# Performance work log

Measured on AMD Instinct MI355X. Metric: run time of the kernel, lower is better.

Reference implementation:

```python
import jax, jax.numpy as jnp
import numpy as np


def setup_inputs() -> dict:
    key = jax.random.key(0)
    k1, k2 = jax.random.split(key)
    B, N, F = 16, 4096, 512
    S, K = 8, 1024          # splits, symbols per codebook
    D = F // S              # sub-vector dim
    x = jax.random.normal(k1, (B, N, F), dtype=jnp.float32)
    # torch init: uniform(-1/symbols, 1/symbols)
    codebooks = jax.random.uniform(k2, (S, K, D), dtype=jnp.float32,
                                   minval=-1.0 / K, maxval=1.0 / K)
    return {"x": x, "codebooks": codebooks}


def reference(x, codebooks):
    B, N, F = x.shape
    S, K, D = codebooks.shape
    xs = x.reshape(B, N, S, D)                       # split into S chunks
    x2 = jnp.sum(xs * xs, axis=-1, keepdims=True)    # [B,N,S,1]
    c2 = jnp.sum(codebooks * codebooks, axis=-1)     # [S,K]
    xc = jnp.einsum('bnsd,skd->bnsk', xs, codebooks)
    dist = x2 + c2[None, None] - 2.0 * xc            # [B,N,S,K]
    idx = jnp.argmin(dist, axis=-1)                  # [B,N,S]
    # gather chosen code vectors per split -> [B,N,S,D]
    sym = codebooks[jnp.arange(S)[None, None, :], idx]
    sg = jax.lax.stop_gradient
    # straight-through quantized output
    quant = (xs + sg(sym - xs)).reshape(B, N, F)
    # per-split mse (mean over B,N,D of each chunk), summed over splits
    dev = (jnp.sum(jnp.mean((sym - sg(xs)) ** 2, axis=(0, 1, 3)))
           + 0.25 * jnp.sum(jnp.mean((xs - sg(sym)) ** 2, axis=(0, 1, 3))))
    return quant, dev
```

## Files before the change

### kernel.cpp

```cpp
#include <hip/hip_runtime.h>
#include <cstdint>

constexpr int Bv = 16, Nv = 4096, Fv = 512, Sv = 8, Kv = 1024, Dv = 64;
constexpr int Mv = Bv * Nv;
#define BDIM 512
constexpr int RG = 4;

using bf16x8 = __attribute__((ext_vector_type(8))) short;
using f32x4  = __attribute__((ext_vector_type(4))) float;
typedef unsigned short u16;
typedef unsigned int u32;

__device__ __forceinline__ u16 bf16rne(float f) {
  union { float f; u32 u; } v; v.f = f;
  u32 u = v.u + 0x7FFFu + ((v.u >> 16) & 1u);
  return (u16)(u >> 16);
}

__device__ __forceinline__ u32 cvtpk(float lo, float hi) {
  u32 r;
  asm("v_cvt_pk_bf16_f32 %0, %1, %2" : "=v"(r) : "v"(lo), "v"(hi));
  return r;
}

__device__ __forceinline__ void gload_lds16(const void* g, void* lds) {
  __builtin_amdgcn_global_load_lds(
      (const __attribute__((address_space(1))) void*)g,
      (__attribute__((address_space(3))) void*)lds, 16, 0, 0);
}
__device__ __forceinline__ void gload_lds4(const void* g, void* lds) {
  __builtin_amdgcn_global_load_lds(
      (const __attribute__((address_space(1))) void*)g,
      (__attribute__((address_space(3))) void*)lds, 4, 0, 0);
}

__global__ void prep_kernel(const float* __restrict__ cb, u16* __restrict__ swz,
                            float* __restrict__ c2m) {
  int idx = blockIdx.x * 256 + threadIdx.x;
  int cw = idx & (Kv - 1);
  const float4* src = (const float4*)(cb + (size_t)idx * Dv);
  float v[64];
  float s2 = 0.f;
#pragma unroll
  for (int i = 0; i < 16; ++i) {
    float4 f = src[i];
    v[i * 4 + 0] = f.x; v[i * 4 + 1] = f.y; v[i * 4 + 2] = f.z; v[i * 4 + 3] = f.w;
    s2 += f.x * f.x + f.y * f.y + f.z * f.z + f.w * f.w;
  }
  c2m[idx] = -0.5f * s2;
  uint4* out = (uint4*)(swz + (size_t)idx * Dv);
#pragma unroll
  for (int slot = 0; slot < 8; ++slot) {
    int slotp = slot ^ (cw & 7);
    u32 w[4];
#pragma unroll
    for (int p = 0; p < 4; ++p)
      w[p] = (u32)bf16rne(v[slot * 8 + p * 2]) | ((u32)bf16rne(v[slot * 8 + p * 2 + 1]) << 16);
    uint4 pk; pk.x = w[0]; pk.y = w[1]; pk.z = w[2]; pk.w = w[3];
    out[slotp] = pk;
  }
}

__global__ __launch_bounds__(BDIM, 2) void pq_mfma(
    const float* __restrict__ x, const float* __restrict__ cb,
    const u16* __restrict__ swz, const float* __restrict__ c2m_g,
    float* __restrict__ quant, float* __restrict__ devpart) {
  __shared__ __attribute__((aligned(16))) u16 cw_lds[Kv * Dv];
  __shared__ __attribute__((aligned(16))) float c2_lds[Kv];

  const int tid = threadIdx.x;
  const int s = blockIdx.x & 7;
  const int chunk = blockIdx.x >> 3;
  const int wave = tid >> 6, lane = tid & 63;
  const int l15 = lane & 15, lg = lane >> 4;
  const int slotp0 = lg ^ (l15 & 7);
  const int slotp1 = (4 + lg) ^ (l15 & 7);

  const u16* swz_s = swz + (size_t)s * Kv * Dv;
#pragma unroll
  for (int it = 0; it < 16; ++it)
    gload_lds16(swz_s + (size_t)(it * BDIM + tid) * 8,
                &cw_lds[(it * BDIM + (tid & ~63)) * 8]);
#pragma unroll
  for (int it = 0; it < 2; ++it)
    gload_lds4(c2m_g + s * Kv + it * BDIM + tid,
               &c2_lds[it * BDIM + (tid & ~63)]);

  float4 xr[RG][4];
  {
    const float* xb = x + (size_t)(chunk * 1024 + wave * 64) * Fv + s * Dv;
#pragma unroll
    for (int rg = 0; rg < RG; ++rg) {
      const float* xp = xb + (size_t)(rg * 16 + l15) * Fv + lg * 8;
      xr[rg][0] = *(const float4*)xp;
      xr[rg][1] = *(const float4*)(xp + 4);
      xr[rg][2] = *(const float4*)(xp + 32);
      xr[rg][3] = *(const float4*)(xp + 36);
    }
  }

  __syncthreads();

  const u16* r0 = cw_lds + l15 * Dv + slotp0 * 8;
  const u16* r1 = cw_lds + l15 * Dv + slotp1 * 8;

  const u32 lgr0 = (u32)(lg * 4), lgr1 = lgr0 | 1u, lgr2 = lgr0 | 2u, lgr3 = lgr0 | 3u;
  float devx2 = 0.f, bvsum = 0.f;

#pragma unroll 1
  for (int u = 0; u < 2; ++u) {
    const int rowu = chunk * 1024 + u * 512 + wave * 64;

    bf16x8 xf[RG][2];
#pragma unroll
    for (int rg = 0; rg < RG; ++rg) {
#pragma unroll
      for (int h = 0; h < 2; ++h) {
        float4 f0 = xr[rg][h * 2], f1 = xr[rg][h * 2 + 1];
        devx2 += f0.x * f0.x + f0.y * f0.y + f0.z * f0.z + f0.w * f0.w
               + f1.x * f1.x + f1.y * f1.y + f1.z * f1.z + f1.w * f1.w;
        union { u32 w[4]; bf16x8 v; } cvt;
        cvt.w[0] = cvtpk(f0.x, f0.y);
        cvt.w[1] = cvtpk(f0.z, f0.w);
        cvt.w[2] = cvtpk(f1.x, f1.y);
        cvt.w[3] = cvtpk(f1.z, f1.w);
        xf[rg][h] = cvt.v;
      }
    }

    float bv[RG];
#pragma unroll
    for (int rg = 0; rg < RG; ++rg) bv[rg] = -3.0e38f;

    bf16x8 aA0, aA1, aB0, aB1, aC0, aC1;
    f32x4 c2A, c2B, c2C;
    f32x4 acc[RG];

    auto readA = [&](int t) {
      aA0 = *(const bf16x8*)(r0 + t * 16 * Dv);
      aA1 = *(const bf16x8*)(r1 + t * 16 * Dv);
      c2A = *(const f32x4*)&c2_lds[t * 16 + lg * 4];
    };
    auto readB = [&](int t) {
      aB0 = *(const bf16x8*)(r0 + t * 16 * Dv);
      aB1 = *(const bf16x8*)(r1 + t * 16 * Dv);
      c2B = *(const f32x4*)&c2_lds[t * 16 + lg * 4];
    };
    auto readC = [&](int t) {
      aC0 = *(const bf16x8*)(r0 + t * 16 * Dv);
      aC1 = *(const bf16x8*)(r1 + t * 16 * Dv);
      c2C = *(const f32x4*)&c2_lds[t * 16 + lg * 4];
    };
    auto mfmaA = [&]() {
      __builtin_amdgcn_s_setprio(1);
#pragma unroll
      for (int rg = 0; rg < RG; ++rg)
        acc[rg] = __builtin_amdgcn_mfma_f32_16x16x32_bf16(aA0, xf[rg][0], c2A, 0, 0, 0);
#pragma unroll
      for (int rg = 0; rg < RG; ++rg)
        acc[rg] = __builtin_amdgcn_mfma_f32_16x16x32_bf16(aA1, xf[rg][1], acc[rg], 0, 0, 0);
      __builtin_amdgcn_s_setprio(0);
    };
    auto mfmaB = [&]() {
      __builtin_amdgcn_s_setprio(1);
#pragma unroll
      for (int rg = 0; rg < RG; ++rg)
        acc[rg] = __builtin_amdgcn_mfma_f32_16x16x32_bf16(aB0, xf[rg][0], c2B, 0, 0, 0);
#pragma unroll
      for (int rg = 0; rg < RG; ++rg)
        acc[rg] = __builtin_amdgcn_mfma_f32_16x16x32_bf16(aB1, xf[rg][1], acc[rg], 0, 0, 0);
      __builtin_amdgcn_s_setprio(0);
    };
    auto mfmaC = [&]() {
      __builtin_amdgcn_s_setprio(1);
#pragma unroll
      for (int rg = 0; rg < RG; ++rg)
        acc[rg] = __builtin_amdgcn_mfma_f32_16x16x32_bf16(aC0, xf[rg][0], c2C, 0, 0, 0);
#pragma unroll
      for (int rg = 0; rg < RG; ++rg)
        acc[rg] = __builtin_amdgcn_mfma_f32_16x16x32_bf16(aC1, xf[rg][1], acc[rg], 0, 0, 0);
      __builtin_amdgcn_s_setprio(0);
    };
    auto proc = [&](u32 tb) {
#pragma unroll
      for (int rg = 0; rg < RG; ++rg) {
        float p0 = __builtin_bit_cast(float, (__builtin_bit_cast(u32, acc[rg][0]) | tb) | lgr0);
        float p1 = __builtin_bit_cast(float, (__builtin_bit_cast(u32, acc[rg][1]) | tb) | lgr1);
        float p2 = __builtin_bit_cast(float, (__builtin_bit_cast(u32, acc[rg][2]) | tb) | lgr2);
        float p3 = __builtin_bit_cast(float, (__builtin_bit_cast(u32, acc[rg][3]) | tb) | lgr3);
        float m = fmaxf(fmaxf(p0, p1), p2);
        bv[rg] = fmaxf(fmaxf(m, p3), bv[rg]);
      }
    };

    readA(0); readB(1); readC(2);
#pragma unroll 1
    for (int k = 0; k < 20; ++k) {
      const int t = 3 * k;
      mfmaA(); readA(t + 3); proc((u32)(t << 4));
      mfmaB(); readB(t + 4); proc((u32)((t + 1) << 4));
      mfmaC(); readC(t + 5); proc((u32)((t + 2) << 4));
    }
    mfmaA(); readA(63); proc(60u << 4);
    mfmaB(); proc(61u << 4);
    mfmaC(); proc(62u << 4);
    mfmaA(); proc(63u << 4);

#pragma unroll
    for (int rg = 0; rg < RG; ++rg) {
      float b = bv[rg];
      b = fmaxf(b, __shfl_xor(b, 16, 64));
      b = fmaxf(b, __shfl_xor(b, 32, 64));
      bv[rg] = b;
      bvsum += b;
    }

    if (u == 0) {
      const float* xb = x + (size_t)(chunk * 1024 + 512 + wave * 64) * Fv + s * Dv;
#pragma unroll
      for (int rg = 0; rg < RG; ++rg) {
        const float* xp = xb + (size_t)(rg * 16 + l15) * Fv + lg * 8;
        xr[rg][0] = *(const float4*)xp;
        xr[rg][1] = *(const float4*)(xp + 4);
        xr[rg][2] = *(const float4*)(xp + 32);
        xr[rg][3] = *(const float4*)(xp + 36);
      }
    }

    const float* cbs = cb + (size_t)s * Kv * Dv;
    float* qbase = quant + (size_t)rowu * Fv + s * Dv;
#pragma unroll
    for (int i = 0; i < 16; ++i) {
      int rl = i * 4 + lg;
      int kk = __shfl(__builtin_bit_cast(int, bv[i >> 2]), 4 * (i & 3) + lg, 64) & 1023;
      f32x4 v = *(const f32x4*)(cbs + (size_t)kk * Dv + l15 * 4);
      __builtin_nontemporal_store(v, (f32x4*)(qbase + (size_t)rl * Fv + l15 * 4));
    }
  }

#pragma unroll
  for (int m = 1; m <= 32; m <<= 1) devx2 += __shfl_xor(devx2, m, 64);
#pragma unroll
  for (int m = 1; m <= 8; m <<= 1) bvsum += __shfl_xor(bvsum, m, 64);
  if (lane == 0)
    devpart[(size_t)blockIdx.x * 8 + wave] = devx2 - 2.f * bvsum;
}

__global__ void dev_reduce(const float* __restrict__ part, float* __restrict__ out) {
  __shared__ float sred[256];
  int tid = threadIdx.x;
  float s = 0.f;
  for (int i = tid; i < 4096; i += 256) s += part[i];
  sred[tid] = s;
  __syncthreads();
  for (int off = 128; off > 0; off >>= 1) {
    if (tid < off) sred[tid] += sred[tid + off];
    __syncthreads();
  }
  if (tid == 0) out[0] = sred[0] * (1.25f / 4194304.0f);
}

extern "C" void kernel_launch(void* const* d_in, const int* in_sizes, int n_in,
                              void* d_out, int out_size, void* d_ws, size_t ws_size,
                              hipStream_t stream) {
  const float* x = (const float*)d_in[0];
  const float* cb = (const float*)d_in[1];
  float* quant = (float*)d_out;
  float* dev = quant + (size_t)Mv * Fv;

  u16* swz = (u16*)d_ws;
  float* c2m = (float*)(swz + (size_t)Sv * Kv * Dv);
  float* part = c2m + Sv * Kv;

  prep_kernel<<<(Sv * Kv) / 256, 256, 0, stream>>>(cb, swz, c2m);
  pq_mfma<<<512, BDIM, 0, stream>>>(x, cb, swz, c2m, quant, part);
  dev_reduce<<<1, 256, 0, stream>>>(part, dev);
}
```

Baseline: 97.97 us.

## Double-buffer MFMA accumulators to overlap argmin processing with next tile

Splits the accumulator into two register sets (P and Q) and restructures the codebook-tile loop so the MFMA cluster for tile t+1 is issued before the max-reduction of tile t's results. Previously each proc step waited on the MFMA just issued into the same registers, serialising matrix and vector work. The loop is unrolled six tiles per iteration with a new prologue and epilogue, which raises VGPR pressure and could lower occupancy.

Result: slower. 100.6 us (+2.7%).

```diff
diff --git a/kernel.cpp b/kernel.cpp
--- a/kernel.cpp
+++ b/kernel.cpp
@@ -134,7 +134,7 @@
 
     bf16x8 aA0, aA1, aB0, aB1, aC0, aC1;
     f32x4 c2A, c2B, c2C;
-    f32x4 acc[RG];
+    f32x4 accP[RG], accQ[RG];
 
     auto readA = [&](int t) {
       aA0 = *(const bf16x8*)(r0 + t * 16 * Dv);
@@ -151,60 +151,60 @@
       aC1 = *(const bf16x8*)(r1 + t * 16 * Dv);
       c2C = *(const f32x4*)&c2_lds[t * 16 + lg * 4];
     };
-    auto mfmaA = [&]() {
-      __builtin_amdgcn_s_setprio(1);
-#pragma unroll
-      for (int rg = 0; rg < RG; ++rg)
-        acc[rg] = __builtin_amdgcn_mfma_f32_16x16x32_bf16(aA0, xf[rg][0], c2A, 0, 0, 0);
-#pragma unroll
-      for (int rg = 0; rg < RG; ++rg)
-        acc[rg] = __builtin_amdgcn_mfma_f32_16x16x32_bf16(aA1, xf[rg][1], acc[rg], 0, 0, 0);
-      __builtin_amdgcn_s_setprio(0);
-    };
-    auto mfmaB = [&]() {
-      __builtin_amdgcn_s_setprio(1);
-#pragma unroll
-      for (int rg = 0; rg < RG; ++rg)
-        acc[rg] = __builtin_amdgcn_mfma_f32_16x16x32_bf16(aB0, xf[rg][0], c2B, 0, 0, 0);
-#pragma unroll
-      for (int rg = 0; rg < RG; ++rg)
-        acc[rg] = __builtin_amdgcn_mfma_f32_16x16x32_bf16(aB1, xf[rg][1], acc[rg], 0, 0, 0);
-      __builtin_amdgcn_s_setprio(0);
-    };
-    auto mfmaC = [&]() {
-      __builtin_amdgcn_s_setprio(1);
-#pragma unroll
-      for (int rg = 0; rg < RG; ++rg)
-        acc[rg] = __builtin_amdgcn_mfma_f32_16x16x32_bf16(aC0, xf[rg][0], c2C, 0, 0, 0);
-#pragma unroll
-      for (int rg = 0; rg < RG; ++rg)
-        acc[rg] = __builtin_amdgcn_mfma_f32_16x16x32_bf16(aC1, xf[rg][1], acc[rg], 0, 0, 0);
-      __builtin_amdgcn_s_setprio(0);
-    };
-    auto proc = [&](u32 tb) {
+
+#define MFMA_CLUSTER(A0, A1, C2, ACC)                                           \
+  do {                                                                          \
+    __builtin_amdgcn_s_setprio(1);                                              \
+    _Pragma("unroll")                                                           \
+    for (int rg = 0; rg < RG; ++rg)                                             \
+      ACC[rg] = __builtin_amdgcn_mfma_f32_16x16x32_bf16(A0, xf[rg][0], C2, 0, 0, 0); \
+    _Pragma("unroll")                                                           \
+    for (int rg = 0; rg < RG; ++rg)                                             \
+      ACC[rg] = __builtin_amdgcn_mfma_f32_16x16x32_bf16(A1, xf[rg][1], ACC[rg], 0, 0, 0); \
+    __builtin_amdgcn_s_setprio(0);                                              \
+  } while (0)
+
+    auto procP = [&](u32 tb) {
 #pragma unroll
       for (int rg = 0; rg < RG; ++rg) {
-        float p0 = __builtin_bit_cast(float, (__builtin_bit_cast(u32, acc[rg][0]) | tb) | lgr0);
-        float p1 = __builtin_bit_cast(float, (__builtin_bit_cast(u32, acc[rg][1]) | tb) | lgr1);
-        float p2 = __builtin_bit_cast(float, (__builtin_bit_cast(u32, acc[rg][2]) | tb) | lgr2);
-        float p3 = __builtin_bit_cast(float, (__builtin_bit_cast(u32, acc[rg][3]) | tb) | lgr3);
+        float p0 = __builtin_bit_cast(float, (__builtin_bit_cast(u32, accP[rg][0]) | tb) | lgr0);
+        float p1 = __builtin_bit_cast(float, (__builtin_bit_cast(u32, accP[rg][1]) | tb) | lgr1);
+        float p2 = __builtin_bit_cast(float, (__builtin_bit_cast(u32, accP[rg][2]) | tb) | lgr2);
+        float p3 = __builtin_bit_cast(float, (__builtin_bit_cast(u32, accP[rg][3]) | tb) | lgr3);
         float m = fmaxf(fmaxf(p0, p1), p2);
         bv[rg] = fmaxf(fmaxf(m, p3), bv[rg]);
       }
     };
+    auto procQ = [&](u32 tb) {
+#pragma unroll
+      for (int rg = 0; rg < RG; ++rg) {
+        float p0 = __builtin_bit_cast(float, (__builtin_bit_cast(u32, accQ[rg][0]) | tb) | lgr0);
+        float p1 = __builtin_bit_cast(float, (__builtin_bit_cast(u32, accQ[rg][1]) | tb) | lgr1);
+        float p2 = __builtin_bit_cast(float, (__builtin_bit_cast(u32, accQ[rg][2]) | tb) | lgr2);
+        float p3 = __builtin_bit_cast(float, (__builtin_bit_cast(u32, accQ[rg][3]) | tb) | lgr3);
+        float m = fmaxf(fmaxf(p0, p1), p2);
+        bv[rg] = fmaxf(fmaxf(m, p3), bv[rg]);
+      }
+    };
 
     readA(0); readB(1); readC(2);
+    MFMA_CLUSTER(aA0, aA1, c2A, accP); readA(3);
 #pragma unroll 1
-    for (int k = 0; k < 20; ++k) {
-      const int t = 3 * k;
-      mfmaA(); readA(t + 3); proc((u32)(t << 4));
-      mfmaB(); readB(t + 4); proc((u32)((t + 1) << 4));
-      mfmaC(); readC(t + 5); proc((u32)((t + 2) << 4));
-    }
-    mfmaA(); readA(63); proc(60u << 4);
-    mfmaB(); proc(61u << 4);
-    mfmaC(); proc(62u << 4);
-    mfmaA(); proc(63u << 4);
+    for (int k = 0; k < 10; ++k) {
+      const int t0 = 6 * k;
+      MFMA_CLUSTER(aB0, aB1, c2B, accQ); readB(t0 + 4); procP((u32)(t0 << 4));
+      MFMA_CLUSTER(aC0, aC1, c2C, accP); readC(t0 + 5); procQ((u32)((t0 + 1) << 4));
+      MFMA_CLUSTER(aA0, aA1, c2A, accQ); readA(t0 + 6); procP((u32)((t0 + 2) << 4));
+      MFMA_CLUSTER(aB0, aB1, c2B, accP); readB(t0 + 7); procQ((u32)((t0 + 3) << 4));
+      MFMA_CLUSTER(aC0, aC1, c2C, accQ); readC(t0 + 8); procP((u32)((t0 + 4) << 4));
+      MFMA_CLUSTER(aA0, aA1, c2A, accP); readA(t0 + 9); procQ((u32)((t0 + 5) << 4));
+    }
+    MFMA_CLUSTER(aB0, aB1, c2B, accQ); procP(60u << 4);
+    MFMA_CLUSTER(aC0, aC1, c2C, accP); procQ(61u << 4);
+    MFMA_CLUSTER(aA0, aA1, c2A, accQ); procP(62u << 4);
+    procQ(63u << 4);
+
+#undef MFMA_CLUSTER
 
 #pragma unroll
     for (int rg = 0; rg < RG; ++rg) {
```

## Switch distance GEMM from 16x16x32 to 32x32x16 MFMA tiles

Applied to the files above, without the earlier changes.

Replaces the 16x16x32 bf16 MFMA tiling with 32x32x16 MFMAs. Each wave now covers 32 codewords by 64 rows per step, using two 16-wide accumulators. The c2 bias array is permuted in the prep kernel to match the 32x32 accumulator layout, and the argmax encoding, shuffle reductions and index gathers are rewritten for the new lane mapping. The aim is fewer MFMA issues and LDS reads per codeword. In exchange there is a longer per-tile max reduction, a single-buffered A prefetch in place of triple buffering, and higher register pressure.

Result: slower. 115.5 us (+17.9%).

```diff
diff --git a/kernel.cpp b/kernel.cpp
--- a/kernel.cpp
+++ b/kernel.cpp
@@ -4,10 +4,10 @@
 constexpr int Bv = 16, Nv = 4096, Fv = 512, Sv = 8, Kv = 1024, Dv = 64;
 constexpr int Mv = Bv * Nv;
 #define BDIM 512
-constexpr int RG = 4;
 
 using bf16x8 = __attribute__((ext_vector_type(8))) short;
 using f32x4  = __attribute__((ext_vector_type(4))) float;
+using f32x16 = __attribute__((ext_vector_type(16))) float;
 typedef unsigned short u16;
 typedef unsigned int u32;
 
@@ -35,9 +35,10 @@
 }
 
 __global__ void prep_kernel(const float* __restrict__ cb, u16* __restrict__ swz,
-                            float* __restrict__ c2m) {
+                            float* __restrict__ c2arr) {
   int idx = blockIdx.x * 256 + threadIdx.x;
   int cw = idx & (Kv - 1);
+  int s = idx >> 10;
   const float4* src = (const float4*)(cb + (size_t)idx * Dv);
   float v[64];
   float s2 = 0.f;
@@ -47,7 +48,12 @@
     v[i * 4 + 0] = f.x; v[i * 4 + 1] = f.y; v[i * 4 + 2] = f.z; v[i * 4 + 3] = f.w;
     s2 += f.x * f.x + f.y * f.y + f.z * f.z + f.w * f.w;
   }
-  c2m[idx] = -0.5f * s2;
+  {
+    int t = cw >> 5, w = cw & 31;
+    int hi = (w >> 2) & 1;
+    int r = (w & 3) | (((w >> 3) & 3) << 2);
+    c2arr[(size_t)s * Kv + t * 32 + hi * 16 + r] = -0.5f * s2;
+  }
   uint4* out = (uint4*)(swz + (size_t)idx * Dv);
 #pragma unroll
   for (int slot = 0; slot < 8; ++slot) {
@@ -63,18 +69,18 @@
 
 __global__ __launch_bounds__(BDIM, 2) void pq_mfma(
     const float* __restrict__ x, const float* __restrict__ cb,
-    const u16* __restrict__ swz, const float* __restrict__ c2m_g,
+    const u16* __restrict__ swz, const float* __restrict__ c2arr_g,
     float* __restrict__ quant, float* __restrict__ devpart) {
   __shared__ __attribute__((aligned(16))) u16 cw_lds[Kv * Dv];
-  __shared__ __attribute__((aligned(16))) float c2_lds[Kv];
+  __shared__ __attribute__((aligned(16))) float c2a_lds[Kv];
 
   const int tid = threadIdx.x;
   const int s = blockIdx.x & 7;
   const int chunk = blockIdx.x >> 3;
   const int wave = tid >> 6, lane = tid & 63;
-  const int l15 = lane & 15, lg = lane >> 4;
-  const int slotp0 = lg ^ (l15 & 7);
-  const int slotp1 = (4 + lg) ^ (l15 & 7);
+  const int m = lane & 31, hi = lane >> 5;
+  const int l15 = lane & 15, lg4 = lane >> 4;
+  const u32 hi4 = (u32)(hi << 2);
 
   const u16* swz_s = swz + (size_t)s * Kv * Dv;
 #pragma unroll
@@ -83,40 +89,40 @@
                 &cw_lds[(it * BDIM + (tid & ~63)) * 8]);
 #pragma unroll
   for (int it = 0; it < 2; ++it)
-    gload_lds4(c2m_g + s * Kv + it * BDIM + tid,
-               &c2_lds[it * BDIM + (tid & ~63)]);
-
-  float4 xr[RG][4];
+    gload_lds4(c2arr_g + (size_t)s * Kv + it * BDIM + tid,
+               &c2a_lds[it * BDIM + (tid & ~63)]);
+
+  float4 xr[2][4][2];
   {
     const float* xb = x + (size_t)(chunk * 1024 + wave * 64) * Fv + s * Dv;
 #pragma unroll
-    for (int rg = 0; rg < RG; ++rg) {
-      const float* xp = xb + (size_t)(rg * 16 + l15) * Fv + lg * 8;
-      xr[rg][0] = *(const float4*)xp;
-      xr[rg][1] = *(const float4*)(xp + 4);
-      xr[rg][2] = *(const float4*)(xp + 32);
-      xr[rg][3] = *(const float4*)(xp + 36);
-    }
+    for (int g = 0; g < 2; ++g)
+#pragma unroll
+      for (int kk = 0; kk < 4; ++kk) {
+        const float* xp = xb + (size_t)(g * 32 + m) * Fv + kk * 16 + hi * 8;
+        xr[g][kk][0] = *(const float4*)xp;
+        xr[g][kk][1] = *(const float4*)(xp + 4);
+      }
   }
 
   __syncthreads();
 
-  const u16* r0 = cw_lds + l15 * Dv + slotp0 * 8;
-  const u16* r1 = cw_lds + l15 * Dv + slotp1 * 8;
-
-  const u32 lgr0 = (u32)(lg * 4), lgr1 = lgr0 | 1u, lgr2 = lgr0 | 2u, lgr3 = lgr0 | 3u;
+  const u16* abase = cw_lds + (size_t)m * Dv;
+  const int sp0 = (0 + hi) ^ (m & 7), sp1 = (2 + hi) ^ (m & 7);
+  const int sp2 = (4 + hi) ^ (m & 7), sp3 = (6 + hi) ^ (m & 7);
+
   float devx2 = 0.f, bvsum = 0.f;
 
 #pragma unroll 1
   for (int u = 0; u < 2; ++u) {
     const int rowu = chunk * 1024 + u * 512 + wave * 64;
 
-    bf16x8 xf[RG][2];
-#pragma unroll
-    for (int rg = 0; rg < RG; ++rg) {
-#pragma unroll
-      for (int h = 0; h < 2; ++h) {
-        float4 f0 = xr[rg][h * 2], f1 = xr[rg][h * 2 + 1];
+    bf16x8 xf[2][4];
+#pragma unroll
+    for (int g = 0; g < 2; ++g)
+#pragma unroll
+      for (int kk = 0; kk < 4; ++kk) {
+        float4 f0 = xr[g][kk][0], f1 = xr[g][kk][1];
         devx2 += f0.x * f0.x + f0.y * f0.y + f0.z * f0.z + f0.w * f0.w
                + f1.x * f1.x + f1.y * f1.y + f1.z * f1.z + f1.w * f1.w;
         union { u32 w[4]; bf16x8 v; } cvt;
@@ -124,124 +130,100 @@
         cvt.w[1] = cvtpk(f0.z, f0.w);
         cvt.w[2] = cvtpk(f1.x, f1.y);
         cvt.w[3] = cvtpk(f1.z, f1.w);
-        xf[rg][h] = cvt.v;
+        xf[g][kk] = cvt.v;
+      }
+
+    float bv0 = -3.0e38f, bv1 = -3.0e38f;
+
+    bf16x8 a0, a1, a2, a3;
+    f32x16 cvv;
+    f32x16 accP, accQ;
+
+    auto readA = [&](int t) {
+      const u16* p = abase + (size_t)t * 32 * Dv;
+      a0 = *(const bf16x8*)(p + sp0 * 8);
+      a1 = *(const bf16x8*)(p + sp1 * 8);
+      a2 = *(const bf16x8*)(p + sp2 * 8);
+      a3 = *(const bf16x8*)(p + sp3 * 8);
+    };
+
+    readA(0);
+#pragma unroll 1
+    for (int t = 0; t < 32; ++t) {
+      cvv = *(const f32x16*)&c2a_lds[t * 32 + hi * 16];
+      __builtin_amdgcn_s_setprio(1);
+      accP = __builtin_amdgcn_mfma_f32_32x32x16_bf16(a0, xf[0][0], cvv, 0, 0, 0);
+      accP = __builtin_amdgcn_mfma_f32_32x32x16_bf16(a1, xf[0][1], accP, 0, 0, 0);
+      accP = __builtin_amdgcn_mfma_f32_32x32x16_bf16(a2, xf[0][2], accP, 0, 0, 0);
+      accP = __builtin_amdgcn_mfma_f32_32x32x16_bf16(a3, xf[0][3], accP, 0, 0, 0);
+      accQ = __builtin_amdgcn_mfma_f32_32x32x16_bf16(a0, xf[1][0], cvv, 0, 0, 0);
+      accQ = __builtin_amdgcn_mfma_f32_32x32x16_bf16(a1, xf[1][1], accQ, 0, 0, 0);
+      accQ = __builtin_amdgcn_mfma_f32_32x32x16_bf16(a2, xf[1][2], accQ, 0, 0, 0);
+      accQ = __builtin_amdgcn_mfma_f32_32x32x16_bf16(a3, xf[1][3], accQ, 0, 0, 0);
+      __builtin_amdgcn_s_setprio(0);
+      if (t < 31) readA(t + 1);
+
+      const u32 tbh = ((u32)t << 5) | hi4;
+      {
+        float p[16];
+#pragma unroll
+        for (int r = 0; r < 16; ++r) {
+          const u32 ruc = (u32)((r & 3) + 8 * (r >> 2));
+          p[r] = __builtin_bit_cast(float, __builtin_bit_cast(u32, accP[r]) | tbh | ruc);
+        }
+#pragma unroll
+        for (int st = 8; st > 0; st >>= 1)
+#pragma unroll
+          for (int r = 0; r < st; ++r) p[r] = fmaxf(p[r], p[r + st]);
+        bv0 = fmaxf(bv0, p[0]);
+      }
+      {
+        float p[16];
+#pragma unroll
+        for (int r = 0; r < 16; ++r) {
+          const u32 ruc = (u32)((r & 3) + 8 * (r >> 2));
+          p[r] = __builtin_bit_cast(float, __builtin_bit_cast(u32, accQ[r]) | tbh | ruc);
+        }
+#pragma unroll
+        for (int st = 8; st > 0; st >>= 1)
+#pragma unroll
+          for (int r = 0; r < st; ++r) p[r] = fmaxf(p[r], p[r + st]);
+        bv1 = fmaxf(bv1, p[0]);
       }
     }
 
-    float bv[RG];
-#pragma unroll
-    for (int rg = 0; rg < RG; ++rg) bv[rg] = -3.0e38f;
-
-    bf16x8 aA0, aA1, aB0, aB1, aC0, aC1;
-    f32x4 c2A, c2B, c2C;
-    f32x4 acc[RG];
-
-    auto readA = [&](int t) {
-      aA0 = *(const bf16x8*)(r0 + t * 16 * Dv);
-      aA1 = *(const bf16x8*)(r1 + t * 16 * Dv);
-      c2A = *(const f32x4*)&c2_lds[t * 16 + lg * 4];
-    };
-    auto readB = [&](int t) {
-      aB0 = *(const bf16x8*)(r0 + t * 16 * Dv);
-      aB1 = *(const bf16x8*)(r1 + t * 16 * Dv);
-      c2B = *(const f32x4*)&c2_lds[t * 16 + lg * 4];
-    };
-    auto readC = [&](int t) {
-      aC0 = *(const bf16x8*)(r0 + t * 16 * Dv);
-      aC1 = *(const bf16x8*)(r1 + t * 16 * Dv);
-      c2C = *(const f32x4*)&c2_lds[t * 16 + lg * 4];
-    };
-    auto mfmaA = [&]() {
-      __builtin_amdgcn_s_setprio(1);
-#pragma unroll
-      for (int rg = 0; rg < RG; ++rg)
-        acc[rg] = __builtin_amdgcn_mfma_f32_16x16x32_bf16(aA0, xf[rg][0], c2A, 0, 0, 0);
-#pragma unroll
-      for (int rg = 0; rg < RG; ++rg)
-        acc[rg] = __builtin_amdgcn_mfma_f32_16x16x32_bf16(aA1, xf[rg][1], acc[rg], 0, 0, 0);
-      __builtin_amdgcn_s_setprio(0);
-    };
-    auto mfmaB = [&]() {
-      __builtin_amdgcn_s_setprio(1);
-#pragma unroll
-      for (int rg = 0; rg < RG; ++rg)
-        acc[rg] = __builtin_amdgcn_mfma_f32_16x16x32_bf16(aB0, xf[rg][0], c2B, 0, 0, 0);
-#pragma unroll
-      for (int rg = 0; rg < RG; ++rg)
-        acc[rg] = __builtin_amdgcn_mfma_f32_16x16x32_bf16(aB1, xf[rg][1], acc[rg], 0, 0, 0);
-      __builtin_amdgcn_s_setprio(0);
-    };
-    auto mfmaC = [&]() {
-      __builtin_amdgcn_s_setprio(1);
-#pragma unroll
-      for (int rg = 0; rg < RG; ++rg)
-        acc[rg] = __builtin_amdgcn_mfma_f32_16x16x32_bf16(aC0, xf[rg][0], c2C, 0, 0, 0);
-#pragma unroll
-      for (int rg = 0; rg < RG; ++rg)
-        acc[rg] = __builtin_amdgcn_mfma_f32_16x16x32_bf16(aC1, xf[rg][1], acc[rg], 0, 0, 0);
-      __builtin_amdgcn_s_setprio(0);
-    };
-    auto proc = [&](u32 tb) {
-#pragma unroll
-      for (int rg = 0; rg < RG; ++rg) {
-        float p0 = __builtin_bit_cast(float, (__builtin_bit_cast(u32, acc[rg][0]) | tb) | lgr0);
-        float p1 = __builtin_bit_cast(float, (__builtin_bit_cast(u32, acc[rg][1]) | tb) | lgr1);
-        float p2 = __builtin_bit_cast(float, (__builtin_bit_cast(u32, acc[rg][2]) | tb) | lgr2);
-        float p3 = __builtin_bit_cast(float, (__builtin_bit_cast(u32, acc[rg][3]) | tb) | lgr3);
-        float m = fmaxf(fmaxf(p0, p1), p2);
-        bv[rg] = fmaxf(fmaxf(m, p3), bv[rg]);
-      }
-    };
-
-    readA(0); readB(1); readC(2);
-#pragma unroll 1
-    for (int k = 0; k < 20; ++k) {
-      const int t = 3 * k;
-      mfmaA(); readA(t + 3); proc((u32)(t << 4));
-      mfmaB(); readB(t + 4); proc((u32)((t + 1) << 4));
-      mfmaC(); readC(t + 5); proc((u32)((t + 2) << 4));
-    }
-    mfmaA(); readA(63); proc(60u << 4);
-    mfmaB(); proc(61u << 4);
-    mfmaC(); proc(62u << 4);
-    mfmaA(); proc(63u << 4);
-
-#pragma unroll
-    for (int rg = 0; rg < RG; ++rg) {
-      float b = bv[rg];
-      b = fmaxf(b, __shfl_xor(b, 16, 64));
-      b = fmaxf(b, __shfl_xor(b, 32, 64));
-      bv[rg] = b;
-      bvsum += b;
-    }
+    bv0 = fmaxf(bv0, __shfl_xor(bv0, 32, 64));
+    bv1 = fmaxf(bv1, __shfl_xor(bv1, 32, 64));
+    bvsum += bv0 + bv1;
 
     if (u == 0) {
       const float* xb = x + (size_t)(chunk * 1024 + 512 + wave * 64) * Fv + s * Dv;
 #pragma unroll
-      for (int rg = 0; rg < RG; ++rg) {
-        const float* xp = xb + (size_t)(rg * 16 + l15) * Fv + lg * 8;
-        xr[rg][0] = *(const float4*)xp;
-        xr[rg][1] = *(const float4*)(xp + 4);
-        xr[rg][2] = *(const float4*)(xp + 32);
-        xr[rg][3] = *(const float4*)(xp + 36);
-      }
+      for (int g = 0; g < 2; ++g)
+#pragma unroll
+        for (int kk = 0; kk < 4; ++kk) {
+          const float* xp = xb + (size_t)(g * 32 + m) * Fv + kk * 16 + hi * 8;
+          xr[g][kk][0] = *(const float4*)xp;
+          xr[g][kk][1] = *(const float4*)(xp + 4);
+        }
     }
 
     const float* cbs = cb + (size_t)s * Kv * Dv;
     float* qbase = quant + (size_t)rowu * Fv + s * Dv;
 #pragma unroll
     for (int i = 0; i < 16; ++i) {
-      int rl = i * 4 + lg;
-      int kk = __shfl(__builtin_bit_cast(int, bv[i >> 2]), 4 * (i & 3) + lg, 64) & 1023;
+      int rl = i * 4 + lg4;
+      float bsel = (i < 8) ? bv0 : bv1;
+      int kk = __shfl(__builtin_bit_cast(int, bsel), rl & 31, 64) & 1023;
       f32x4 v = *(const f32x4*)(cbs + (size_t)kk * Dv + l15 * 4);
       __builtin_nontemporal_store(v, (f32x4*)(qbase + (size_t)rl * Fv + l15 * 4));
     }
   }
 
 #pragma unroll
-  for (int m = 1; m <= 32; m <<= 1) devx2 += __shfl_xor(devx2, m, 64);
-#pragma unroll
-  for (int m = 1; m <= 8; m <<= 1) bvsum += __shfl_xor(bvsum, m, 64);
+  for (int mm = 1; mm <= 32; mm <<= 1) devx2 += __shfl_xor(devx2, mm, 64);
+#pragma unroll
+  for (int mm = 1; mm <= 16; mm <<= 1) bvsum += __shfl_xor(bvsum, mm, 64);
   if (lane == 0)
     devpart[(size_t)blockIdx.x * 8 + wave] = devx2 - 2.f * bvsum;
 }
@@ -269,10 +251,10 @@
   float* dev = quant + (size_t)Mv * Fv;
 
   u16* swz = (u16*)d_ws;
-  float* c2m = (float*)(swz + (size_t)Sv * Kv * Dv);
-  float* part = c2m + Sv * Kv;
-
-  prep_kernel<<<(Sv * Kv) / 256, 256, 0, stream>>>(cb, swz, c2m);
-  pq_mfma<<<512, BDIM, 0, stream>>>(x, cb, swz, c2m, quant, part);
+  float* c2arr = (float*)(swz + (size_t)Sv * Kv * Dv);
+  float* part = c2arr + Sv * Kv;
+
+  prep_kernel<<<(Sv * Kv) / 256, 256, 0, stream>>>(cb, swz, c2arr);
+  pq_mfma<<<512, BDIM, 0, stream>>>(x, cb, swz, c2arr, quant, part);
   dev_reduce<<<1, 256, 0, stream>>>(part, dev);
 }
```
